# Kernel optimization log

Hardware: AMD Instinct MI355X
Metric: run time of the kernel (lower is better)

Reference implementation:

```python
import jax, jax.numpy as jnp
import numpy as np

B, D_IN, H, DIM, K = 16384, 2000, 500, 64, 256
DELTA = -5.0


def _xavier(key, shape):
    fan_out, fan_in = shape
    lim = jnp.sqrt(6.0 / (fan_in + fan_out))
    return jax.random.uniform(key, shape, jnp.float32, -lim, lim)


def setup_inputs() -> dict:
    key = jax.random.key(0)
    ks = jax.random.split(key, 8)
    return {
        "epoch": 0,
        "pre_iter": 0,
        "x": jax.random.uniform(ks[0], (B, D_IN), jnp.float32),
        "mu": jax.random.normal(ks[1], (K, DIM), jnp.float32),
        "enc_w1": _xavier(ks[2], (H, D_IN)), "enc_b1": jnp.zeros((H,), jnp.float32),
        "enc_w2": _xavier(ks[3], (DIM, H)), "enc_b2": jnp.zeros((DIM,), jnp.float32),
        "fc0_w": _xavier(ks[4], (DIM, 2 * DIM)), "fc0_b": jnp.zeros((DIM,), jnp.float32),
        "dec_w1": _xavier(ks[5], (H, DIM)), "dec_b1": jnp.zeros((H,), jnp.float32),
        "dec_w2": _xavier(ks[6], (D_IN, H)), "dec_b2": jnp.zeros((D_IN,), jnp.float32),
    }


def reference(epoch, pre_iter, x, mu, enc_w1, enc_b1, enc_w2, enc_b2,
              fc0_w, fc0_b, dec_w1, dec_b1, dec_w2, dec_b2):
    # encoder (Dropout is identity in eval)
    h = jax.nn.relu(x @ enc_w1.T + enc_b1)            # [B, 500]
    z = h @ enc_w2.T + enc_b2                          # [B, dim]
    # Stein_IMG clustering step (mu is detached in the original)
    mu_d = jax.lax.stop_gradient(mu)
    diff = z[:, None, :] - mu_d[None, :, :]           # [B, K, dim]
    z_dist = jnp.mean(diff * diff, axis=2)            # [B, K]
    gamma = jax.nn.softmax(DELTA * z_dist, axis=1)    # [B, K]
    idx = jnp.argmax(gamma, axis=1)                   # [B]
    # one-hot scatter + matmul with mu == gather of nearest centroid
    quantized = mu_d[idx]                             # [B, dim]
    double_z = jnp.concatenate([z, quantized], axis=1)  # [B, 2*dim]
    recon_z = double_z @ fc0_w.T + fc0_b              # [B, dim]
    # decoder
    h2 = jax.nn.relu(recon_z @ dec_w1.T + dec_b1)     # [B, 500]
    recon_x = jax.nn.sigmoid(h2 @ dec_w2.T + dec_b2)  # [B, 2000]
    return (z, quantized, gamma, recon_x)
```

## Files before the change

### kernel.cpp

```cpp
#include <hip/hip_runtime.h>
#include <stdint.h>
#include <math.h>

#define NB   16384
#define DIN  2000
#define NH   500
#define ND   64
#define NKC  256

#define FLAG_CAP 4096
#define GAP_THR  0.002f

typedef __attribute__((ext_vector_type(4))) float  f32x4;
typedef __attribute__((ext_vector_type(4))) double f64x4;
typedef __attribute__((ext_vector_type(8))) short  s16x8;

__device__ __forceinline__ unsigned short f2bf_rne(float v) {
  unsigned int u = __float_as_uint(v);
  u += 0x7fffu + ((u >> 16) & 1u);
  return (unsigned short)(u >> 16);
}
__device__ __forceinline__ void split_rtz(float v, unsigned short &hi, unsigned short &lo) {
  unsigned int u = __float_as_uint(v);
  hi = (unsigned short)(u >> 16);
  float r = v - __uint_as_float(u & 0xffff0000u);
  lo = (unsigned short)(__float_as_uint(r) >> 16);
}

typedef const __attribute__((address_space(1))) void* gas_t;
typedef __attribute__((address_space(3))) void* las_t;
__device__ __forceinline__ void gl_lds16(const void* g, void* l) {
  __builtin_amdgcn_global_load_lds((gas_t)g, (las_t)l, 16, 0, 0);
}

__device__ __forceinline__ void split_pad_seg(const float* __restrict__ in,
                                              unsigned short* __restrict__ hi,
                                              unsigned short* __restrict__ lo,
                                              int R, int C, int Cp, int total,
                                              int bseg, int nblk) {
  int stride = nblk * 256;
  for (int idx = bseg * 256 + threadIdx.x; idx < total; idx += stride) {
    int r = idx / Cp, c = idx - r * Cp;
    float v = (r < R && c < C) ? in[(size_t)r * C + c] : 0.f;
    if (lo) {
      unsigned short h, l; split_rtz(v, h, l);
      hi[idx] = h; lo[idx] = l;
    } else {
      hi[idx] = f2bf_rne(v);
    }
  }
}

__global__ __launch_bounds__(256) void k_prep(const float* __restrict__ w1,
                                              unsigned short* __restrict__ W1HI,
                                              unsigned short* __restrict__ W1LO,
                                              const float* __restrict__ w2,
                                              unsigned short* __restrict__ W2HI,
                                              unsigned short* __restrict__ W2LO,
                                              const float* __restrict__ dw1,
                                              unsigned short* __restrict__ DW1,
                                              const float* __restrict__ dw2,
                                              unsigned short* __restrict__ DW2,
                                              int* __restrict__ fcnt)
{
  const int b = blockIdx.x;
  if (b == 0 && threadIdx.x == 0) *fcnt = 0;
  if (b < 1024) {
    split_pad_seg(w1, W1HI, W1LO, 500, 2000, 2048, 512 * 2048, b, 1024);
  } else if (b < 1088) {
    split_pad_seg(w2, W2HI, W2LO, 64, 500, 512, 64 * 512, b - 1024, 64);
  } else if (b < 1152) {
    split_pad_seg(dw1, DW1, nullptr, 500, 64, 64, 512 * 64, b - 1088, 64);
  } else {
    split_pad_seg(dw2, DW2, nullptr, 2000, 500, 512, 2048 * 512, b - 1152, 896);
  }
}

template<int WR, int BN, int WC, bool SPLIT, bool AF32, int EPI, int BK>
__global__ __launch_bounds__(256) void k_gemm(
    const unsigned short* __restrict__ Ahi, const unsigned short* __restrict__ Alo,
    const float* __restrict__ Axf,
    const unsigned short* __restrict__ Bhi, const unsigned short* __restrict__ Blo,
    const float* __restrict__ bias, int bias_n,
    void* __restrict__ out0, void* __restrict__ out1,
    int ldA, int K, int out_ld, int store_n)
{
  constexpr int BM  = WR * 32;
  constexpr int CPR = BK / 8;
  constexpr int ACH = BM * CPR;
  constexpr int BCH = BN * CPR;
  __shared__ unsigned short aHi[BM * BK];
  __shared__ unsigned short aLo[SPLIT ? BM * BK : 8];
  __shared__ unsigned short bHi[BN * BK];
  __shared__ unsigned short bLo[SPLIT ? BN * BK : 8];

  const int tid  = threadIdx.x;
  const int lane = tid & 63, wave = tid >> 6;
  const int wm = wave >> 1, wn = wave & 1;
  const int lr = lane & 15, lg = lane >> 4;
  const int swz = (lr >> 1) & (CPR - 1);
  const int m0 = blockIdx.x * BM, n0 = blockIdx.y * BN;

  f32x4 acc[WR][WC];
#pragma unroll
  for (int i = 0; i < WR; ++i)
#pragma unroll
    for (int j = 0; j < WC; ++j)
#pragma unroll
      for (int r = 0; r < 4; ++r) acc[i][j][r] = 0.f;

  for (int k0 = 0; k0 < K; k0 += BK) {
#pragma unroll
    for (int j = 0; j < ACH / 256; ++j) {
      int c = (j * 4 + wave) * 64 + lane;
      int row = c / CPR;
      int ch = (c & (CPR - 1)) ^ ((row >> 1) & (CPR - 1));
      if constexpr (AF32) {
        int col = k0 + ch * 8;
        s16x8 h8 = {0,0,0,0,0,0,0,0}, l8 = {0,0,0,0,0,0,0,0};
        if (col < DIN) {
          const float* src = Axf + (size_t)(m0 + row) * ldA + col;
          f32x4 v0 = *(const f32x4*)src;
          f32x4 v1 = *(const f32x4*)(src + 4);
#pragma unroll
          for (int q = 0; q < 4; ++q) {
            unsigned short h, l;
            split_rtz(v0[q], h, l); h8[q] = (short)h; l8[q] = (short)l;
            split_rtz(v1[q], h, l); h8[4 + q] = (short)h; l8[4 + q] = (short)l;
          }
        }
        *(s16x8*)&aHi[c * 8] = h8;
        *(s16x8*)&aLo[c * 8] = l8;
      } else {
        const unsigned short* sA = Ahi + (size_t)(m0 + row) * ldA + k0 + ch * 8;
        gl_lds16(sA, (char*)aHi + c * 16);
        if constexpr (SPLIT) {
          const unsigned short* sL = Alo + (size_t)(m0 + row) * ldA + k0 + ch * 8;
          gl_lds16(sL, (char*)aLo + c * 16);
        }
      }
    }
#pragma unroll
    for (int j = 0; j < BCH / 256; ++j) {
      int c = (j * 4 + wave) * 64 + lane;
      int row = c / CPR;
      int ch = (c & (CPR - 1)) ^ ((row >> 1) & (CPR - 1));
      const unsigned short* sB = Bhi + (size_t)(n0 + row) * K + k0 + ch * 8;
      gl_lds16(sB, (char*)bHi + c * 16);
      if constexpr (SPLIT) {
        const unsigned short* sL = Blo + (size_t)(n0 + row) * K + k0 + ch * 8;
        gl_lds16(sL, (char*)bLo + c * 16);
      }
    }
    __syncthreads();

#pragma unroll
    for (int kk = 0; kk < BK / 32; ++kk) {
      const int fch = ((lg + 4 * kk) ^ swz) << 3;
      s16x8 ah[WR], bh[WC];
#pragma unroll
      for (int i = 0; i < WR; ++i)
        ah[i] = *(const s16x8*)&aHi[(wm * (WR * 16) + i * 16 + lr) * BK + fch];
#pragma unroll
      for (int j = 0; j < WC; ++j)
        bh[j] = *(const s16x8*)&bHi[(wn * (WC * 16) + j * 16 + lr) * BK + fch];
      if constexpr (SPLIT) {
        s16x8 al[WR], bl[WC];
#pragma unroll
        for (int i = 0; i < WR; ++i)
          al[i] = *(const s16x8*)&aLo[(wm * (WR * 16) + i * 16 + lr) * BK + fch];
#pragma unroll
        for (int j = 0; j < WC; ++j)
          bl[j] = *(const s16x8*)&bLo[(wn * (WC * 16) + j * 16 + lr) * BK + fch];
#pragma unroll
        for (int i = 0; i < WR; ++i)
#pragma unroll
          for (int j = 0; j < WC; ++j) {
            acc[i][j] = __builtin_amdgcn_mfma_f32_16x16x32_bf16(ah[i], bh[j], acc[i][j], 0, 0, 0);
            acc[i][j] = __builtin_amdgcn_mfma_f32_16x16x32_bf16(ah[i], bl[j], acc[i][j], 0, 0, 0);
            acc[i][j] = __builtin_amdgcn_mfma_f32_16x16x32_bf16(al[i], bh[j], acc[i][j], 0, 0, 0);
          }
      } else {
#pragma unroll
        for (int i = 0; i < WR; ++i)
#pragma unroll
          for (int j = 0; j < WC; ++j)
            acc[i][j] = __builtin_amdgcn_mfma_f32_16x16x32_bf16(ah[i], bh[j], acc[i][j], 0, 0, 0);
      }
    }
    __syncthreads();
  }

#pragma unroll
  for (int i = 0; i < WR; ++i) {
    int grow = m0 + wm * (WR * 16) + i * 16 + lg * 4;
#pragma unroll
    for (int j = 0; j < WC; ++j) {
      int gcol = n0 + wn * (WC * 16) + j * 16 + lr;
      float bv = (gcol < bias_n) ? bias[gcol] : 0.f;
      f32x4 v = acc[i][j];
#pragma unroll
      for (int r = 0; r < 4; ++r) {
        float val = v[r] + bv;
        int rr = grow + r;
        if constexpr (EPI == 0) {
          if (gcol < store_n) ((float*)out0)[(size_t)rr * out_ld + gcol] = val;
        } else if constexpr (EPI == 1) {
          val = fmaxf(val, 0.f);
          unsigned short h, l; split_rtz(val, h, l);
          ((unsigned short*)out0)[(size_t)rr * out_ld + gcol] = h;
          ((unsigned short*)out1)[(size_t)rr * out_ld + gcol] = l;
        } else if constexpr (EPI == 2) {
          val = fmaxf(val, 0.f);
          ((unsigned short*)out0)[(size_t)rr * out_ld + gcol] = f2bf_rne(val);
        } else {
          val = 1.f / (1.f + expf(-val));
          if (gcol < store_n) ((float*)out0)[(size_t)rr * out_ld + gcol] = val;
        }
      }
    }
  }
}

__global__ __launch_bounds__(256) void k_cluster(const float* __restrict__ z,
                                                 const float* __restrict__ mu,
                                                 float* __restrict__ gamma,
                                                 float* __restrict__ quant,
                                                 int* __restrict__ flag_cnt,
                                                 int* __restrict__ flag_list)
{
  __shared__ float mu_t[ND][NKC];
  for (int i = threadIdx.x; i < NKC * ND; i += 256) {
    int k = i >> 6, d = i & 63;
    mu_t[d][k] = mu[i];
  }
  __syncthreads();
  const int lane = threadIdx.x & 63, wave = threadIdx.x >> 6;
  for (int r4 = blockIdx.x * 16 + wave * 4; r4 < NB; r4 += gridDim.x * 16) {
    float zr[4];
#pragma unroll
    for (int r = 0; r < 4; ++r) zr[r] = z[(size_t)(r4 + r) * ND + lane];
    float ds[4][4];
#pragma unroll
    for (int r = 0; r < 4; ++r)
#pragma unroll
      for (int g = 0; g < 4; ++g) ds[r][g] = 0.f;
    for (int d = 0; d < ND; ++d) {
      f32x4 m4 = *(const f32x4*)&mu_t[d][lane << 2];
#pragma unroll
      for (int r = 0; r < 4; ++r) {
        float zd = __shfl(zr[r], d, 64);
#pragma unroll
        for (int g = 0; g < 4; ++g) {
          float t = zd - m4[g];
          ds[r][g] = fmaf(t, t, ds[r][g]);
        }
      }
    }
#pragma unroll
    for (int r = 0; r < 4; ++r) {
      int row = r4 + r;
      float bd = ds[r][0]; int bk = (lane << 2);
#pragma unroll
      for (int g = 1; g < 4; ++g)
        if (ds[r][g] < bd) { bd = ds[r][g]; bk = (lane << 2) + g; }
      for (int off = 1; off < 64; off <<= 1) {
        float od = __shfl_xor(bd, off, 64);
        int   ok = __shfl_xor(bk, off, 64);
        if (od < bd || (od == bd && ok < bk)) { bd = od; bk = ok; }
      }
      float sb = 3.4e38f;
#pragma unroll
      for (int g = 0; g < 4; ++g) {
        int kk = (lane << 2) + g;
        if (kk != bk) sb = fminf(sb, ds[r][g]);
      }
      for (int off = 1; off < 64; off <<= 1) sb = fminf(sb, __shfl_xor(sb, off, 64));
      if (lane == 0 && (sb - bd) < GAP_THR) {
        int p = atomicAdd(flag_cnt, 1);
        if (p < FLAG_CAP) flag_list[p] = row;
      }
      const float cc = -5.f / 64.f;
      float e[4], s = 0.f;
#pragma unroll
      for (int g = 0; g < 4; ++g) { e[g] = expf(cc * (ds[r][g] - bd)); s += e[g]; }
      for (int off = 1; off < 64; off <<= 1) s += __shfl_xor(s, off, 64);
      float inv = 1.f / s;
      f32x4 g4 = { e[0] * inv, e[1] * inv, e[2] * inv, e[3] * inv };
      *(f32x4*)&gamma[(size_t)row * NKC + (lane << 2)] = g4;
      quant[(size_t)row * ND + lane] = mu[(size_t)bk * ND + lane];
    }
  }
}

__global__ __launch_bounds__(512) void k_ref_h(const float* __restrict__ x,
                                               const float* __restrict__ w1,
                                               const float* __restrict__ b1,
                                               const int* __restrict__ flag_cnt,
                                               const int* __restrict__ flag_list,
                                               double* __restrict__ Hd)
{
  __shared__ __align__(16) double xs[2][DIN];
  __shared__ int rows_s[2];

  int cnt = *flag_cnt; if (cnt > FLAG_CAP) cnt = FLAG_CAP;
  const int base = blockIdx.x * 2;
  if (base >= cnt) return;
  const int tid = threadIdx.x, lane = tid & 63, wave = tid >> 6;
  const int ybase = blockIdx.y * 64;
  const int yend  = (ybase + 64 < NH) ? (ybase + 64) : NH;

  if (tid < 2) rows_s[tid] = flag_list[(base + tid < cnt) ? (base + tid) : base];
  __syncthreads();
  const int row0 = rows_s[0], row1 = rows_s[1];

  for (int c = tid; c < DIN; c += 512) {
    xs[0][c] = (double)x[(size_t)row0 * DIN + c];
    xs[1][c] = (double)x[(size_t)row1 * DIN + c];
  }
  __syncthreads();

  for (int hr0 = ybase + wave * 4; hr0 < yend; hr0 += 32) {
    double a[4][2];
#pragma unroll
    for (int r = 0; r < 4; ++r) { a[r][0] = 0.0; a[r][1] = 0.0; }
    for (int c = lane; c < DIN / 4; c += 64) {
      f64x4 x0 = *(const f64x4*)(&xs[0][c * 4]);
      f64x4 x1 = *(const f64x4*)(&xs[1][c * 4]);
#pragma unroll
      for (int r = 0; r < 4; ++r) {
        f32x4 w4 = *(const f32x4*)(w1 + (size_t)(hr0 + r) * DIN + c * 4);
#pragma unroll
        for (int j = 0; j < 4; ++j) {
          double w = (double)w4[j];
          a[r][0] = fma(w, x0[j], a[r][0]);
          a[r][1] = fma(w, x1[j], a[r][1]);
        }
      }
    }
#pragma unroll
    for (int off = 32; off; off >>= 1)
#pragma unroll
      for (int r = 0; r < 4; ++r) {
        a[r][0] += __shfl_xor(a[r][0], off, 64);
        a[r][1] += __shfl_xor(a[r][1], off, 64);
      }
    if (lane == 0) {
#pragma unroll
      for (int r = 0; r < 4; ++r) {
        double b = (double)b1[hr0 + r];
        double v0 = a[r][0] + b, v1 = a[r][1] + b;
        Hd[(size_t)(base + 0) * 512 + hr0 + r] = v0 > 0.0 ? v0 : 0.0;
        Hd[(size_t)(base + 1) * 512 + hr0 + r] = v1 > 0.0 ? v1 : 0.0;
      }
    }
  }
}

__global__ __launch_bounds__(512) void k_ref_zq(const float* __restrict__ w2,
                                                const float* __restrict__ b2,
                                                const float* __restrict__ mu,
                                                const double* __restrict__ Hd,
                                                const int* __restrict__ flag_cnt,
                                                const int* __restrict__ flag_list,
                                                float* __restrict__ quant)
{
  __shared__ double hsl[8][NH];
  __shared__ float  mu_t[ND][NKC + 1];
  __shared__ double zs[8][ND];
  __shared__ int    rows_s[8];

  int cnt = *flag_cnt; if (cnt > FLAG_CAP) cnt = FLAG_CAP;
  const int base = blockIdx.x * 8;
  if (base >= cnt) return;
  const int tid = threadIdx.x, lane = tid & 63, wave = tid >> 6;

  if (tid < 8) rows_s[tid] = flag_list[(base + tid < cnt) ? (base + tid) : base];
  for (int i = tid; i < NKC * ND; i += 512) {
    mu_t[i & 63][i >> 6] = mu[i];
  }
  {
    int pos = (base + wave < cnt) ? (base + wave) : base;
    const double* hr = Hd + (size_t)pos * 512;
    for (int i = lane; i < NH; i += 64) hsl[wave][i] = hr[i];
  }
  __syncthreads();

  for (int g4 = 0; g4 < 16; ++g4) {
    double a[4] = {0.0, 0.0, 0.0, 0.0};
    int q[4];
#pragma unroll
    for (int u = 0; u < 4; ++u) q[u] = g4 * 32 + u * 8 + wave;
    for (int i = lane; i < NH; i += 64) {
#pragma unroll
      for (int u = 0; u < 4; ++u) {
        int r = q[u] >> 6, d = q[u] & 63;
        a[u] = fma(hsl[r][i], (double)w2[(size_t)d * NH + i], a[u]);
      }
    }
#pragma unroll
    for (int off = 32; off; off >>= 1)
#pragma unroll
      for (int u = 0; u < 4; ++u) a[u] += __shfl_xor(a[u], off, 64);
    if (lane == 0) {
#pragma unroll
      for (int u = 0; u < 4; ++u) {
        int r = q[u] >> 6, d = q[u] & 63;
        zs[r][d] = a[u] + (double)b2[d];
      }
    }
  }
  __syncthreads();

  {
    double bd = 1.0e300; int bk = 0;
#pragma unroll
    for (int g = 0; g < 4; ++g) {
      int k = g * 64 + lane;
      double dist = 0.0;
#pragma unroll 8
      for (int d = 0; d < ND; ++d) {
        double t = zs[wave][d] - (double)mu_t[d][k];
        dist = fma(t, t, dist);
      }
      if (g == 0 || dist < bd) { bd = dist; bk = k; }
    }
    for (int off = 1; off < 64; off <<= 1) {
      double od = __shfl_xor(bd, off, 64);
      int    ok = __shfl_xor(bk, off, 64);
      if (od < bd || (od == bd && ok < bk)) { bd = od; bk = ok; }
    }
    quant[(size_t)rows_s[wave] * ND + lane] = mu[(size_t)bk * ND + lane];
  }
}

__global__ __launch_bounds__(256) void k_fc0(const float* __restrict__ z, const float* __restrict__ quant,
                                             const float* __restrict__ W, const float* __restrict__ b,
                                             unsigned short* __restrict__ rz)
{
  __shared__ float Wt[2 * ND][ND];
  for (int i = threadIdx.x; i < ND * 2 * ND; i += 256) {
    int j = i >> 7;
    int ii = i & 127;
    Wt[ii][j] = W[i];
  }
  __syncthreads();
  const int lane = threadIdx.x & 63, wave = threadIdx.x >> 6;
  float bj = b[lane];
  for (int row = blockIdx.x * 4 + wave; row < NB; row += gridDim.x * 4) {
    float zv = z[(size_t)row * ND + lane];
    float qv = quant[(size_t)row * ND + lane];
    float acc = bj;
#pragma unroll 8
    for (int i = 0; i < ND; ++i) {
      acc = fmaf(__shfl(zv, i, 64), Wt[i][lane], acc);
      acc = fmaf(__shfl(qv, i, 64), Wt[ND + i][lane], acc);
    }
    rz[(size_t)row * ND + lane] = f2bf_rne(acc);
  }
}

extern "C" void kernel_launch(void* const* d_in, const int* in_sizes, int n_in,
                              void* d_out, int out_size, void* d_ws, size_t ws_size,
                              hipStream_t stream)
{
  const float* x      = (const float*)d_in[2];
  const float* mu     = (const float*)d_in[3];
  const float* enc_w1 = (const float*)d_in[4];
  const float* enc_b1 = (const float*)d_in[5];
  const float* enc_w2 = (const float*)d_in[6];
  const float* enc_b2 = (const float*)d_in[7];
  const float* fc0_w  = (const float*)d_in[8];
  const float* fc0_b  = (const float*)d_in[9];
  const float* dec_w1 = (const float*)d_in[10];
  const float* dec_b1 = (const float*)d_in[11];
  const float* dec_w2 = (const float*)d_in[12];
  const float* dec_b2 = (const float*)d_in[13];

  float* z_out  = (float*)d_out;
  float* q_out  = z_out + (size_t)NB * ND;
  float* g_out  = q_out + (size_t)NB * ND;
  float* rx_out = g_out + (size_t)NB * NKC;

  char* ws = (char*)d_ws;
  unsigned short* W1HI = (unsigned short*)ws; ws += (size_t)512 * 2048 * 2;
  unsigned short* W1LO = (unsigned short*)ws; ws += (size_t)512 * 2048 * 2;
  unsigned short* W2HI = (unsigned short*)ws; ws += (size_t)64 * 512 * 2;
  unsigned short* W2LO = (unsigned short*)ws; ws += (size_t)64 * 512 * 2;
  unsigned short* DW1  = (unsigned short*)ws; ws += (size_t)512 * 64 * 2;
  unsigned short* DW2  = (unsigned short*)ws; ws += (size_t)2048 * 512 * 2;
  unsigned short* HHI  = (unsigned short*)ws; ws += (size_t)NB * 512 * 2;
  unsigned short* HLO  = (unsigned short*)ws; ws += (size_t)NB * 512 * 2;
  unsigned short* H2   = (unsigned short*)ws; ws += (size_t)NB * 512 * 2;
  unsigned short* RZ   = (unsigned short*)ws; ws += (size_t)NB * ND * 2;
  int* FCNT = (int*)ws; ws += 256;
  int* FLST = (int*)ws; ws += (size_t)FLAG_CAP * 4;
  double* Hd = (double*)ws; ws += (size_t)FLAG_CAP * 512 * 8;

  k_prep<<<2048, 256, 0, stream>>>(enc_w1, W1HI, W1LO, enc_w2, W2HI, W2LO,
                                   dec_w1, DW1, dec_w2, DW2, FCNT);

  dim3 g1(NB / 128, 4);
  k_gemm<4, 128, 4, true, true, 1, 64><<<g1, 256, 0, stream>>>(
      nullptr, nullptr, x, W1HI, W1LO, enc_b1, 500, HHI, HLO, DIN, 2048, 512, 512);
  dim3 g2(NB / 64, 1);
  k_gemm<2, 64, 2, true, false, 0, 32><<<g2, 256, 0, stream>>>(
      HHI, HLO, nullptr, W2HI, W2LO, enc_b2, 64, z_out, nullptr, 512, 512, 64, 64);
  k_cluster<<<256, 256, 0, stream>>>(z_out, mu, g_out, q_out, FCNT, FLST);
  dim3 gh(FLAG_CAP / 2, 8);
  k_ref_h<<<gh, 512, 0, stream>>>(x, enc_w1, enc_b1, FCNT, FLST, Hd);
  k_ref_zq<<<FLAG_CAP / 8, 512, 0, stream>>>(enc_w2, enc_b2, mu, Hd, FCNT, FLST, q_out);
  k_fc0<<<256, 256, 0, stream>>>(z_out, q_out, fc0_w, fc0_b, RZ);
  dim3 g4(NB / 128, 4);
  k_gemm<4, 128, 4, false, false, 2, 32><<<g4, 256, 0, stream>>>(
      RZ, nullptr, nullptr, DW1, nullptr, dec_b1, 500, H2, nullptr, 64, 64, 512, 512);
  dim3 g5(NB / 128, 16);
  k_gemm<4, 128, 4, false, false, 3, 32><<<g5, 256, 0, stream>>>(
      H2, nullptr, nullptr, DW2, nullptr, dec_b2, 2000, rx_out, nullptr, 512, 512, 2000, 2000);
}
```

Before: 372.8 us.

## Fuse encoder second GEMM with clustering step; raise decoder GEMM K-tile

Merges the z = h·W2ᵀ GEMM (split-bf16, three MFMA passes) and the clustering/argmin kernel into one kernel. Each block computes a 64-row tile of z, stages it in LDS and runs the distance/softmax/argmin step directly, which removes a launch and the global reread of z. The decoder GEMMs also get a larger K-tile template parameter (32 to 64). The fused kernel uses far more LDS (mu transpose plus the A/B tiles plus z), which may cut occupancy, and it reloads mu into LDS in every one of the 256 blocks.

Result: faster. 356.8 us (-4.3%).

```diff
diff --git a/kernel.cpp b/kernel.cpp
--- a/kernel.cpp
+++ b/kernel.cpp
@@ -222,24 +222,108 @@
   }
 }
 
-__global__ __launch_bounds__(256) void k_cluster(const float* __restrict__ z,
-                                                 const float* __restrict__ mu,
-                                                 float* __restrict__ gamma,
-                                                 float* __restrict__ quant,
-                                                 int* __restrict__ flag_cnt,
-                                                 int* __restrict__ flag_list)
+__global__ __launch_bounds__(256) void k_gemm2c(
+    const unsigned short* __restrict__ Ahi, const unsigned short* __restrict__ Alo,
+    const unsigned short* __restrict__ Bhi, const unsigned short* __restrict__ Blo,
+    const float* __restrict__ bias,
+    const float* __restrict__ mu,
+    float* __restrict__ z, float* __restrict__ gamma, float* __restrict__ quant,
+    int* __restrict__ flag_cnt, int* __restrict__ flag_list)
 {
+  constexpr int BM = 64, BN = 64, BK = 64, CPR = 8, WR = 2, WC = 2, K = 512;
+  __shared__ unsigned short aHi[BM * BK];
+  __shared__ unsigned short aLo[BM * BK];
+  __shared__ unsigned short bHi[BN * BK];
+  __shared__ unsigned short bLo[BN * BK];
+  __shared__ float zl[64][64];
   __shared__ float mu_t[ND][NKC];
-  for (int i = threadIdx.x; i < NKC * ND; i += 256) {
-    int k = i >> 6, d = i & 63;
-    mu_t[d][k] = mu[i];
+
+  const int tid  = threadIdx.x;
+  const int lane = tid & 63, wave = tid >> 6;
+  const int wm = wave >> 1, wn = wave & 1;
+  const int lr = lane & 15, lg = lane >> 4;
+  const int swz = (lr >> 1) & (CPR - 1);
+  const int m0 = blockIdx.x * BM;
+
+  for (int i = tid; i < NKC * ND; i += 256) {
+    mu_t[i & 63][i >> 6] = mu[i];
+  }
+
+  f32x4 acc[WR][WC];
+#pragma unroll
+  for (int i = 0; i < WR; ++i)
+#pragma unroll
+    for (int j = 0; j < WC; ++j)
+#pragma unroll
+      for (int r = 0; r < 4; ++r) acc[i][j][r] = 0.f;
+
+  for (int k0 = 0; k0 < K; k0 += BK) {
+#pragma unroll
+    for (int j = 0; j < (BM * CPR) / 256; ++j) {
+      int c = (j * 4 + wave) * 64 + lane;
+      int row = c / CPR;
+      int ch = (c & (CPR - 1)) ^ ((row >> 1) & (CPR - 1));
+      gl_lds16(Ahi + (size_t)(m0 + row) * K + k0 + ch * 8, (char*)aHi + c * 16);
+      gl_lds16(Alo + (size_t)(m0 + row) * K + k0 + ch * 8, (char*)aLo + c * 16);
+    }
+#pragma unroll
+    for (int j = 0; j < (BN * CPR) / 256; ++j) {
+      int c = (j * 4 + wave) * 64 + lane;
+      int row = c / CPR;
+      int ch = (c & (CPR - 1)) ^ ((row >> 1) & (CPR - 1));
+      gl_lds16(Bhi + (size_t)row * K + k0 + ch * 8, (char*)bHi + c * 16);
+      gl_lds16(Blo + (size_t)row * K + k0 + ch * 8, (char*)bLo + c * 16);
+    }
+    __syncthreads();
+#pragma unroll
+    for (int kk = 0; kk < BK / 32; ++kk) {
+      const int fch = ((lg + 4 * kk) ^ swz) << 3;
+      s16x8 ah[WR], bh[WC], al[WR], bl[WC];
+#pragma unroll
+      for (int i = 0; i < WR; ++i) {
+        ah[i] = *(const s16x8*)&aHi[(wm * 32 + i * 16 + lr) * BK + fch];
+        al[i] = *(const s16x8*)&aLo[(wm * 32 + i * 16 + lr) * BK + fch];
+      }
+#pragma unroll
+      for (int j = 0; j < WC; ++j) {
+        bh[j] = *(const s16x8*)&bHi[(wn * 32 + j * 16 + lr) * BK + fch];
+        bl[j] = *(const s16x8*)&bLo[(wn * 32 + j * 16 + lr) * BK + fch];
+      }
+#pragma unroll
+      for (int i = 0; i < WR; ++i)
+#pragma unroll
+        for (int j = 0; j < WC; ++j) {
+          acc[i][j] = __builtin_amdgcn_mfma_f32_16x16x32_bf16(ah[i], bh[j], acc[i][j], 0, 0, 0);
+          acc[i][j] = __builtin_amdgcn_mfma_f32_16x16x32_bf16(ah[i], bl[j], acc[i][j], 0, 0, 0);
+          acc[i][j] = __builtin_amdgcn_mfma_f32_16x16x32_bf16(al[i], bh[j], acc[i][j], 0, 0, 0);
+        }
+    }
+    __syncthreads();
+  }
+
+#pragma unroll
+  for (int i = 0; i < WR; ++i) {
+    int lrow = wm * 32 + i * 16 + lg * 4;
+#pragma unroll
+    for (int j = 0; j < WC; ++j) {
+      int col = wn * 32 + j * 16 + lr;
+      float bv = bias[col];
+      f32x4 v = acc[i][j];
+#pragma unroll
+      for (int r = 0; r < 4; ++r) {
+        float val = v[r] + bv;
+        z[(size_t)(m0 + lrow + r) * ND + col] = val;
+        zl[lrow + r][col] = val;
+      }
+    }
   }
   __syncthreads();
-  const int lane = threadIdx.x & 63, wave = threadIdx.x >> 6;
-  for (int r4 = blockIdx.x * 16 + wave * 4; r4 < NB; r4 += gridDim.x * 16) {
+
+  for (int it = 0; it < 4; ++it) {
+    int r4 = wave * 16 + it * 4;
     float zr[4];
 #pragma unroll
-    for (int r = 0; r < 4; ++r) zr[r] = z[(size_t)(r4 + r) * ND + lane];
+    for (int r = 0; r < 4; ++r) zr[r] = zl[r4 + r][lane];
     float ds[4][4];
 #pragma unroll
     for (int r = 0; r < 4; ++r)
@@ -259,7 +343,7 @@
     }
 #pragma unroll
     for (int r = 0; r < 4; ++r) {
-      int row = r4 + r;
+      int row = m0 + r4 + r;
       float bd = ds[r][0]; int bk = (lane << 2);
 #pragma unroll
       for (int g = 1; g < 4; ++g)
@@ -503,18 +587,16 @@
   dim3 g1(NB / 128, 4);
   k_gemm<4, 128, 4, true, true, 1, 64><<<g1, 256, 0, stream>>>(
       nullptr, nullptr, x, W1HI, W1LO, enc_b1, 500, HHI, HLO, DIN, 2048, 512, 512);
-  dim3 g2(NB / 64, 1);
-  k_gemm<2, 64, 2, true, false, 0, 32><<<g2, 256, 0, stream>>>(
-      HHI, HLO, nullptr, W2HI, W2LO, enc_b2, 64, z_out, nullptr, 512, 512, 64, 64);
-  k_cluster<<<256, 256, 0, stream>>>(z_out, mu, g_out, q_out, FCNT, FLST);
+  k_gemm2c<<<NB / 64, 256, 0, stream>>>(HHI, HLO, W2HI, W2LO, enc_b2, mu,
+                                        z_out, g_out, q_out, FCNT, FLST);
   dim3 gh(FLAG_CAP / 2, 8);
   k_ref_h<<<gh, 512, 0, stream>>>(x, enc_w1, enc_b1, FCNT, FLST, Hd);
   k_ref_zq<<<FLAG_CAP / 8, 512, 0, stream>>>(enc_w2, enc_b2, mu, Hd, FCNT, FLST, q_out);
   k_fc0<<<256, 256, 0, stream>>>(z_out, q_out, fc0_w, fc0_b, RZ);
   dim3 g4(NB / 128, 4);
-  k_gemm<4, 128, 4, false, false, 2, 32><<<g4, 256, 0, stream>>>(
+  k_gemm<4, 128, 4, false, false, 2, 64><<<g4, 256, 0, stream>>>(
       RZ, nullptr, nullptr, DW1, nullptr, dec_b1, 500, H2, nullptr, 64, 64, 512, 512);
   dim3 g5(NB / 128, 16);
-  k_gemm<4, 128, 4, false, false, 3, 32><<<g5, 256, 0, stream>>>(
+  k_gemm<4, 128, 4, false, false, 3, 64><<<g5, 256, 0, stream>>>(
       H2, nullptr, nullptr, DW2, nullptr, dec_b2, 2000, rx_out, nullptr, 512, 512, 2000, 2000);
 }
```
